# Kernel tuning notes

Measured on AMD Instinct MI355X. Metric: run time of the kernel, lower is better.

## Reference

```python
import jax, jax.numpy as jnp
import numpy as np

B, T, D_IN = 32, 1000, 1024
H = 32          # hidden_size
G = 4 * H       # gate dim (i,f,g,o)
L = 4           # num_layers


def setup_inputs() -> dict:
    key = jax.random.key(0)
    ks = jax.random.split(key, 12)
    s = 1.0 / np.sqrt(H)  # PyTorch LSTM init scale
    inp = {
        'x': jax.random.normal(ks[0], (B, T, D_IN), dtype=jnp.float32),
        # layer 0 (input dim 1024), [dir, ...]
        'w_ih0': jax.random.uniform(ks[1], (2, G, D_IN), minval=-s, maxval=s),
        'w_hh0': jax.random.uniform(ks[2], (2, G, H), minval=-s, maxval=s),
        'b_ih0': jax.random.uniform(ks[3], (2, G), minval=-s, maxval=s),
        'b_hh0': jax.random.uniform(ks[4], (2, G), minval=-s, maxval=s),
        # layers 1..3 (input dim 2H=64), [layer, dir, ...]
        'w_ih': jax.random.uniform(ks[5], (L - 1, 2, G, 2 * H), minval=-s, maxval=s),
        'w_hh': jax.random.uniform(ks[6], (L - 1, 2, G, H), minval=-s, maxval=s),
        'b_ih': jax.random.uniform(ks[7], (L - 1, 2, G), minval=-s, maxval=s),
        'b_hh': jax.random.uniform(ks[8], (L - 1, 2, G), minval=-s, maxval=s),
        # fc: Linear(64, 1)
        'fc_w': jax.random.uniform(ks[9], (1, 2 * H), minval=-0.125, maxval=0.125),
        'fc_b': jax.random.uniform(ks[10], (1,), minval=-0.125, maxval=0.125),
    }
    return inp


def _lstm_dir(x, wi, wh, b, reverse):
    # x: [B,T,Din]; wi: [4H,Din]; wh: [4H,H]; b: [4H]
    xp = jnp.einsum('btd,gd->tbg', x, wi) + b  # precomputed input proj [T,B,4H]
    whT = wh.T

    def step(carry, xt):
        h, c = carry
        g = xt + h @ whT
        i, f, gg, o = jnp.split(g, 4, axis=-1)  # PyTorch gate order i,f,g,o
        c = jax.nn.sigmoid(f) * c + jax.nn.sigmoid(i) * jnp.tanh(gg)
        h = jax.nn.sigmoid(o) * jnp.tanh(c)
        return (h, c), h

    init = (jnp.zeros((x.shape[0], H), x.dtype), jnp.zeros((x.shape[0], H), x.dtype))
    _, hs = jax.lax.scan(step, init, xp, reverse=reverse)  # hs aligned with input time order
    return hs.transpose(1, 0, 2)  # [B,T,H]


def _bilstm(x, wi, wh, bi, bh):
    fwd = _lstm_dir(x, wi[0], wh[0], bi[0] + bh[0], False)
    bwd = _lstm_dir(x, wi[1], wh[1], bi[1] + bh[1], True)
    return jnp.concatenate([fwd, bwd], axis=-1)  # [B,T,2H]


def reference(x, w_ih0, w_hh0, b_ih0, b_hh0, w_ih, w_hh, b_ih, b_hh, fc_w, fc_b):
    h = _bilstm(x, w_ih0, w_hh0, b_ih0, b_hh0)
    for l in range(L - 1):
        h = _bilstm(h, w_ih[l], w_hh[l], b_ih[l], b_hh[l])
    pooled = h.mean(axis=-2)           # [B,2H]
    return pooled @ fc_w.T + fc_b      # [B,1]
```

## Files before the change

kernel.cpp:

```cpp
#include <hip/hip_runtime.h>


#define TB 1000
#define LOG2E 1.44269504088896340736f

typedef int   v2i __attribute__((ext_vector_type(2)));
typedef float v2f __attribute__((ext_vector_type(2)));

__device__ __forceinline__ float fexp2(float x) {
#if __has_builtin(__builtin_amdgcn_exp2f)
    return __builtin_amdgcn_exp2f(x);
#else
    return exp2f(x);
#endif
}

__device__ __forceinline__ float lane_xor32(float v, bool pickx) {
    v2i r = __builtin_amdgcn_permlane32_swap(__float_as_int(v), __float_as_int(v),
                                             false, false);
    return __int_as_float(pickx ? r[0] : r[1]);
}

__global__ __launch_bounds__(256)
void gemm_proj(const float* __restrict__ A, int K,
               const float* __restrict__ W,
               const float* __restrict__ bi,
               const float* __restrict__ bh,
               float* __restrict__ xpT)
{
    __shared__ __align__(16) float As[32][68];
    __shared__ __align__(16) float Bs[32][132];

    const int tid = threadIdx.x;
    const int m0 = blockIdx.x * 64;
    const int n0 = blockIdx.y * 128;
    const int tx = tid & 15;
    const int ty = tid >> 4;

    float acc[8][4];
#pragma unroll
    for (int i = 0; i < 8; ++i)
#pragma unroll
        for (int jj = 0; jj < 4; ++jj) acc[i][jj] = 0.0f;

    const int ar = tid >> 3;
    const int ak = (tid & 7) * 4;
    const int wr = tid >> 1;
    const int wk = (tid & 1) * 16;

    for (int k0 = 0; k0 < K; k0 += 32) {
        float4 a0 = *(const float4*)(A + (size_t)(m0 + ar) * K + k0 + ak);
        float4 a1 = *(const float4*)(A + (size_t)(m0 + ar + 32) * K + k0 + ak);
        const float* wp = W + (size_t)(n0 + wr) * K + k0 + wk;
        float4 w0 = *(const float4*)(wp + 0);
        float4 w1 = *(const float4*)(wp + 4);
        float4 w2 = *(const float4*)(wp + 8);
        float4 w3 = *(const float4*)(wp + 12);

        __syncthreads();
        As[ak + 0][ar] = a0.x; As[ak + 1][ar] = a0.y;
        As[ak + 2][ar] = a0.z; As[ak + 3][ar] = a0.w;
        As[ak + 0][ar + 32] = a1.x; As[ak + 1][ar + 32] = a1.y;
        As[ak + 2][ar + 32] = a1.z; As[ak + 3][ar + 32] = a1.w;
        {
            float wv[16] = {w0.x, w0.y, w0.z, w0.w,
                            w1.x, w1.y, w1.z, w1.w,
                            w2.x, w2.y, w2.z, w2.w,
                            w3.x, w3.y, w3.z, w3.w};
#pragma unroll
            for (int q = 0; q < 16; ++q) Bs[wk + q][wr] = wv[q];
        }
        __syncthreads();

#pragma unroll
        for (int kk = 0; kk < 32; ++kk) {
            float4 av = *(const float4*)&As[kk][tx * 4];
            float4 b0 = *(const float4*)&Bs[kk][ty * 8];
            float4 b1 = *(const float4*)&Bs[kk][ty * 8 + 4];
            float bn[8] = {b0.x, b0.y, b0.z, b0.w, b1.x, b1.y, b1.z, b1.w};
#pragma unroll
            for (int ni = 0; ni < 8; ++ni) {
                acc[ni][0] = fmaf(av.x, bn[ni], acc[ni][0]);
                acc[ni][1] = fmaf(av.y, bn[ni], acc[ni][1]);
                acc[ni][2] = fmaf(av.z, bn[ni], acc[ni][2]);
                acc[ni][3] = fmaf(av.w, bn[ni], acc[ni][3]);
            }
        }
    }

    const int dir = n0 >> 7;
    const int mbase = m0 + tx * 4;
    const int bidx = mbase / 1000;
    const int ttq = mbase - bidx * 1000;
#pragma unroll
    for (int ni = 0; ni < 8; ++ni) {
        const int n = n0 + ty * 8 + ni;
        const float bias = bi[n] + bh[n];
        const float sc = (((n >> 5) & 3) == 2) ? (-2.0f * LOG2E) : (-LOG2E);
        float* row = xpT + ((size_t)((dir * 32 + bidx) * 128) + (n & 127)) * TB;
        if (dir == 0) {
            float4 o = {(acc[ni][0] + bias) * sc, (acc[ni][1] + bias) * sc,
                        (acc[ni][2] + bias) * sc, (acc[ni][3] + bias) * sc};
            *(float4*)(row + ttq) = o;
        } else {
            float4 o = {(acc[ni][3] + bias) * sc, (acc[ni][2] + bias) * sc,
                        (acc[ni][1] + bias) * sc, (acc[ni][0] + bias) * sc};
            *(float4*)(row + (TB - 4 - ttq)) = o;
        }
    }
}

template<int MODE>
__global__ __launch_bounds__(64)
void lstm_rec(const float* __restrict__ xpT,
              const float* __restrict__ whh,
              float* __restrict__ hout,
              float* __restrict__ hsum)
{
    __shared__ __align__(16) float hsh[32];

    const int blk  = blockIdx.x;
    const int dir  = blk >> 5;
    const int b    = blk & 31;
    const int lane = threadIdx.x & 63;
    const int j    = lane & 31;
    const int up   = lane >> 5;
    const int r0   = j + up * 64;
    const int r1   = r0 + 32;

    v2i det = __builtin_amdgcn_permlane32_swap(lane, lane, false, false);
    const bool pickx = (det[0] == (lane ^ 32));

    const float sA = up ? (-2.0f * LOG2E) : (-LOG2E);
    const float sB = -LOG2E;
    v2f wa[16], wb[16];
    {
        const float* wp0 = whh + (size_t)(dir * 128 + r0) * 32;
        const float* wp1 = whh + (size_t)(dir * 128 + r1) * 32;
#pragma unroll
        for (int q = 0; q < 8; ++q) {
            float4 v = *(const float4*)(wp0 + q * 4);
            wa[2 * q + 0][0] = v.x * sA; wa[2 * q + 0][1] = v.y * sA;
            wa[2 * q + 1][0] = v.z * sA; wa[2 * q + 1][1] = v.w * sA;
            float4 u = *(const float4*)(wp1 + q * 4);
            wb[2 * q + 0][0] = u.x * sB; wb[2 * q + 0][1] = u.y * sB;
            wb[2 * q + 1][0] = u.z * sB; wb[2 * q + 1][1] = u.w * sB;
        }
    }

    const float* pa = xpT + ((size_t)blk * 128 + r0) * TB;
    const float* pb = xpT + ((size_t)blk * 128 + r1) * TB;

    float4 A0 = *(const float4*)(pa + 0);
    float4 B0 = *(const float4*)(pb + 0);
    float4 A1 = *(const float4*)(pa + 4);
    float4 B1 = *(const float4*)(pb + 4);

    const float mA = up ?  2.0f : 1.0f;
    const float mB = up ? -1.0f : 0.0f;

    float c = 0.0f, h = 0.0f, hacc = 0.0f;
    float* hq = hout + ((size_t)b * TB + (dir ? TB - 1 : 0)) * 64 + dir * 32 + j;
    const int hstep = dir ? -64 : 64;

    const unsigned lds_z  = (unsigned)(size_t)&hsh[0];
    const unsigned lds_wa = lds_z + 4u * (unsigned)j;

    float4 hv0, hv1, hv2, hv3, hv4v, hv5, hv6, hv7;

#define DS_WRITE_H() \
    asm volatile("ds_write_b32 %0, %1" :: "v"(lds_wa), "v"(h))

#define DS_ISSUE_READS() do {                                                   \
    asm volatile("ds_read_b128 %0, %1 offset:0"   : "=v"(hv0)  : "v"(lds_z));   \
    asm volatile("ds_read_b128 %0, %1 offset:16"  : "=v"(hv1)  : "v"(lds_z));   \
    asm volatile("ds_read_b128 %0, %1 offset:32"  : "=v"(hv2)  : "v"(lds_z));   \
    asm volatile("ds_read_b128 %0, %1 offset:48"  : "=v"(hv3)  : "v"(lds_z));   \
    asm volatile("ds_read_b128 %0, %1 offset:64"  : "=v"(hv4v) : "v"(lds_z));   \
    asm volatile("ds_read_b128 %0, %1 offset:80"  : "=v"(hv5)  : "v"(lds_z));   \
    asm volatile("ds_read_b128 %0, %1 offset:96"  : "=v"(hv6)  : "v"(lds_z));   \
    asm volatile("ds_read_b128 %0, %1 offset:112" : "=v"(hv7)  : "v"(lds_z));   \
    } while (0)

#define MVG(HV, CNT, I0, I1, Q)                                                 \
    asm volatile("s_waitcnt lgkmcnt(" #CNT ")");                                \
    __builtin_amdgcn_sched_barrier(0);                                          \
    {                                                                           \
        v2f h0_ = {HV.x, HV.y};                                                 \
        v2f h1_ = {HV.z, HV.w};                                                 \
        qa[I0] = __builtin_elementwise_fma(h0_, wa[2*Q],   qa[I0]);             \
        qb[I0] = __builtin_elementwise_fma(h0_, wb[2*Q],   qb[I0]);             \
        qa[I1] = __builtin_elementwise_fma(h1_, wa[2*Q+1], qa[I1]);             \
        qb[I1] = __builtin_elementwise_fma(h1_, wb[2*Q+1], qb[I1]);             \
    }

    DS_WRITE_H();
    DS_ISSUE_READS();

#define LSTM_STEP(GA, GB) do {                                                  \
        v2f qa[4], qb[4];                                                       \
        qa[0] = v2f{(GA), 0.0f}; qa[1] = v2f{0.f, 0.f};                         \
        qa[2] = v2f{0.f, 0.f};   qa[3] = v2f{0.f, 0.f};                         \
        qb[0] = v2f{(GB), 0.0f}; qb[1] = v2f{0.f, 0.f};                         \
        qb[2] = v2f{0.f, 0.f};   qb[3] = v2f{0.f, 0.f};                         \
        MVG(hv0,  7, 0, 1, 0)                                                   \
        MVG(hv1,  6, 2, 3, 1)                                                   \
        MVG(hv2,  5, 0, 1, 2)                                                   \
        MVG(hv3,  4, 2, 3, 3)                                                   \
        MVG(hv4v, 3, 0, 1, 4)                                                   \
        MVG(hv5,  2, 2, 3, 5)                                                   \
        MVG(hv6,  1, 0, 1, 6)                                                   \
        MVG(hv7,  0, 2, 3, 7)                                                   \
        v2f sa = (qa[0] + qa[2]) + (qa[1] + qa[3]);                             \
        v2f sb = (qb[0] + qb[2]) + (qb[1] + qb[3]);                             \
        float g0 = sa[0] + sa[1];                                               \
        float g1 = sb[0] + sb[1];                                               \
        float s0 = __builtin_amdgcn_rcpf(1.0f + fexp2(g0));                     \
        float v0 = fmaf(mA, s0, mB);               \
        float v1 = __builtin_amdgcn_rcpf(1.0f + fexp2(g1));  \
        float o0 = lane_xor32(v0, pickx);                                       \
        float o1 = lane_xor32(v1, pickx);                                       \
        float P  = v0 * o0;                        \
        float sf = up ? o1 : v1;                                                \
        float so = up ? v1 : o1;                                                \
        c = fmaf(sf, c, P);                                                     \
        float tc = fmaf(2.0f, __builtin_amdgcn_rcpf(1.0f + fexp2(c * (-2.0f * LOG2E))), -1.0f); \
        h = so * tc;                                                            \
        DS_WRITE_H();                                                           \
        DS_ISSUE_READS();                                                       \
        if (MODE == 0) {                                                        \
            asm volatile("global_store_dword %0, %1, off" :: "v"(hq), "v"(h));  \
        } else {                                                                \
            hacc += h;                                                          \
        }                                                                       \
        hq += hstep;                                                            \
    } while (0)

    for (int it = 0; it < 125; ++it) {
        const int base = it * 8;
        const int offn0 = min(base + 8,  TB - 4);
        const int offn1 = min(base + 12, TB - 4);
        float4 NA0 = *(const float4*)(pa + offn0);
        float4 NB0 = *(const float4*)(pb + offn0);
        float4 NA1 = *(const float4*)(pa + offn1);
        float4 NB1 = *(const float4*)(pb + offn1);

        LSTM_STEP(A0.x, B0.x);
        LSTM_STEP(A0.y, B0.y);
        LSTM_STEP(A0.z, B0.z);
        LSTM_STEP(A0.w, B0.w);
        LSTM_STEP(A1.x, B1.x);
        LSTM_STEP(A1.y, B1.y);
        LSTM_STEP(A1.z, B1.z);
        LSTM_STEP(A1.w, B1.w);

        A0 = NA0; B0 = NB0; A1 = NA1; B1 = NB1;
    }
#undef LSTM_STEP
#undef MVG
#undef DS_ISSUE_READS
#undef DS_WRITE_H

    asm volatile("s_waitcnt lgkmcnt(0)" ::: "memory");

    if (MODE == 1) hsum[b * 64 + dir * 32 + j] = hacc;
}

__global__ __launch_bounds__(64)
void final_fc(const float* __restrict__ hsum,
              const float* __restrict__ fcw,
              const float* __restrict__ fcb,
              float* __restrict__ out)
{
    int b = blockIdx.x;
    int l = threadIdx.x;
    float v = hsum[b * 64 + l] * (1.0f / (float)TB) * fcw[l];
#pragma unroll
    for (int off = 32; off > 0; off >>= 1)
        v += __shfl_down(v, off, 64);
    if (l == 0) out[b] = v + fcb[0];
}

extern "C" void kernel_launch(void* const* d_in, const int* in_sizes, int n_in,
                              void* d_out, int out_size, void* d_ws, size_t ws_size,
                              hipStream_t stream)
{
    const float* x    = (const float*)d_in[0];
    const float* wih0 = (const float*)d_in[1];
    const float* whh0 = (const float*)d_in[2];
    const float* bih0 = (const float*)d_in[3];
    const float* bhh0 = (const float*)d_in[4];
    const float* wih  = (const float*)d_in[5];
    const float* whh  = (const float*)d_in[6];
    const float* bih  = (const float*)d_in[7];
    const float* bhh  = (const float*)d_in[8];
    const float* fcw  = (const float*)d_in[9];
    const float* fcb  = (const float*)d_in[10];
    float* out = (float*)d_out;

    float* ws = (float*)d_ws;
    float* xp = ws;
    float* hb = ws + 8192000;
    float* hs = ws + 8192000 + 2048000;

    dim3 gb(500, 2);

    gemm_proj<<<gb, 256, 0, stream>>>(x, 1024, wih0, bih0, bhh0, xp);
    lstm_rec<0><<<64, 64, 0, stream>>>(xp, whh0, hb, hs);

    for (int l = 1; l < 4; ++l) {
        const float* wl  = wih + (size_t)(l - 1) * 2 * 128 * 64;
        const float* whl = whh + (size_t)(l - 1) * 2 * 128 * 32;
        const float* b1  = bih + (size_t)(l - 1) * 256;
        const float* b2  = bhh + (size_t)(l - 1) * 256;
        gemm_proj<<<gb, 256, 0, stream>>>(hb, 64, wl, b1, b2, xp);
        if (l == 3) lstm_rec<1><<<64, 64, 0, stream>>>(xp, whl, hb, hs);
        else        lstm_rec<0><<<64, 64, 0, stream>>>(xp, whl, hb, hs);
    }

    final_fc<<<32, 64, 0, stream>>>(hs, fcw, fcb, out);
}
```

Baseline: 1.033 ms.

## Double-buffer projection GEMM and read first h lanes via readlane

The input-projection GEMM now uses two LDS buffers, so the next K-chunk's global loads overlap the current chunk's FMAs and one barrier per iteration is removed. In the recurrent LSTM step, the first 8 hidden values come from v_readlane of the wave's own h register into SGPRs and feed packed FMAs, replacing two LDS reads on the serial critical path. The aim is to shorten per-timestep latency. The inline asm clobbers fixed SGPRs s64-s71, and it relies on lanes 0-7 holding h[0..7]. That holds only if this wave produced those lanes.

```diff
diff --git a/kernel.cpp b/kernel.cpp
--- a/kernel.cpp
+++ b/kernel.cpp
@@ -28,8 +28,8 @@
                const float* __restrict__ bh,
                float* __restrict__ xpT)
 {
-    __shared__ __align__(16) float As[32][68];
-    __shared__ __align__(16) float Bs[32][132];
+    __shared__ __align__(16) float As[2][32][72];
+    __shared__ __align__(16) float Bs[2][32][132];
 
     const int tid = threadIdx.x;
     const int m0 = blockIdx.x * 64;
@@ -37,46 +37,54 @@
     const int tx = tid & 15;
     const int ty = tid >> 4;
 
-    float acc[8][4];
-#pragma unroll
-    for (int i = 0; i < 8; ++i)
-#pragma unroll
-        for (int jj = 0; jj < 4; ++jj) acc[i][jj] = 0.0f;
+    float acc[8][4] = {};
 
     const int ar = tid >> 3;
     const int ak = (tid & 7) * 4;
     const int wr = tid >> 1;
     const int wk = (tid & 1) * 16;
 
-    for (int k0 = 0; k0 < K; k0 += 32) {
-        float4 a0 = *(const float4*)(A + (size_t)(m0 + ar) * K + k0 + ak);
-        float4 a1 = *(const float4*)(A + (size_t)(m0 + ar + 32) * K + k0 + ak);
-        const float* wp = W + (size_t)(n0 + wr) * K + k0 + wk;
-        float4 w0 = *(const float4*)(wp + 0);
-        float4 w1 = *(const float4*)(wp + 4);
-        float4 w2 = *(const float4*)(wp + 8);
-        float4 w3 = *(const float4*)(wp + 12);
-
-        __syncthreads();
-        As[ak + 0][ar] = a0.x; As[ak + 1][ar] = a0.y;
-        As[ak + 2][ar] = a0.z; As[ak + 3][ar] = a0.w;
-        As[ak + 0][ar + 32] = a1.x; As[ak + 1][ar + 32] = a1.y;
-        As[ak + 2][ar + 32] = a1.z; As[ak + 3][ar + 32] = a1.w;
-        {
-            float wv[16] = {w0.x, w0.y, w0.z, w0.w,
-                            w1.x, w1.y, w1.z, w1.w,
-                            w2.x, w2.y, w2.z, w2.w,
-                            w3.x, w3.y, w3.z, w3.w};
-#pragma unroll
-            for (int q = 0; q < 16; ++q) Bs[wk + q][wr] = wv[q];
-        }
-        __syncthreads();
+    const float* Abase = A + (size_t)(m0 + ar) * K + ak;
+    const float* Wbase = W + (size_t)(n0 + wr) * K + wk;
+
+    float4 a0 = *(const float4*)(Abase);
+    float4 a1 = *(const float4*)(Abase + (size_t)32 * K);
+    float4 w0 = *(const float4*)(Wbase + 0);
+    float4 w1 = *(const float4*)(Wbase + 4);
+    float4 w2 = *(const float4*)(Wbase + 8);
+    float4 w3 = *(const float4*)(Wbase + 12);
+
+    {
+        As[0][ak + 0][ar] = a0.x; As[0][ak + 1][ar] = a0.y;
+        As[0][ak + 2][ar] = a0.z; As[0][ak + 3][ar] = a0.w;
+        As[0][ak + 0][ar + 32] = a1.x; As[0][ak + 1][ar + 32] = a1.y;
+        As[0][ak + 2][ar + 32] = a1.z; As[0][ak + 3][ar + 32] = a1.w;
+        float wv[16] = {w0.x, w0.y, w0.z, w0.w, w1.x, w1.y, w1.z, w1.w,
+                        w2.x, w2.y, w2.z, w2.w, w3.x, w3.y, w3.z, w3.w};
+#pragma unroll
+        for (int q = 0; q < 16; ++q) Bs[0][wk + q][wr] = wv[q];
+    }
+    __syncthreads();
+
+    const int nch = K >> 5;
+    int p = 0;
+    for (int ch = 0; ch < nch; ++ch) {
+        const bool more = (ch + 1 < nch);
+        if (more) {
+            const int k0 = (ch + 1) * 32;
+            a0 = *(const float4*)(Abase + k0);
+            a1 = *(const float4*)(Abase + (size_t)32 * K + k0);
+            w0 = *(const float4*)(Wbase + k0);
+            w1 = *(const float4*)(Wbase + k0 + 4);
+            w2 = *(const float4*)(Wbase + k0 + 8);
+            w3 = *(const float4*)(Wbase + k0 + 12);
+        }
 
 #pragma unroll
         for (int kk = 0; kk < 32; ++kk) {
-            float4 av = *(const float4*)&As[kk][tx * 4];
-            float4 b0 = *(const float4*)&Bs[kk][ty * 8];
-            float4 b1 = *(const float4*)&Bs[kk][ty * 8 + 4];
+            float4 av = *(const float4*)&As[p][kk][tx * 4];
+            float4 b0 = *(const float4*)&Bs[p][kk][ty * 8];
+            float4 b1 = *(const float4*)&Bs[p][kk][ty * 8 + 4];
             float bn[8] = {b0.x, b0.y, b0.z, b0.w, b1.x, b1.y, b1.z, b1.w};
 #pragma unroll
             for (int ni = 0; ni < 8; ++ni) {
@@ -86,6 +94,20 @@
                 acc[ni][3] = fmaf(av.w, bn[ni], acc[ni][3]);
             }
         }
+
+        if (more) {
+            const int np = p ^ 1;
+            As[np][ak + 0][ar] = a0.x; As[np][ak + 1][ar] = a0.y;
+            As[np][ak + 2][ar] = a0.z; As[np][ak + 3][ar] = a0.w;
+            As[np][ak + 0][ar + 32] = a1.x; As[np][ak + 1][ar + 32] = a1.y;
+            As[np][ak + 2][ar + 32] = a1.z; As[np][ak + 3][ar + 32] = a1.w;
+            float wv[16] = {w0.x, w0.y, w0.z, w0.w, w1.x, w1.y, w1.z, w1.w,
+                            w2.x, w2.y, w2.z, w2.w, w3.x, w3.y, w3.z, w3.w};
+#pragma unroll
+            for (int q = 0; q < 16; ++q) Bs[np][wk + q][wr] = wv[q];
+            __syncthreads();
+        }
+        p ^= 1;
     }
 
     const int dir = n0 >> 7;
@@ -166,14 +188,12 @@
     const unsigned lds_z  = (unsigned)(size_t)&hsh[0];
     const unsigned lds_wa = lds_z + 4u * (unsigned)j;
 
-    float4 hv0, hv1, hv2, hv3, hv4v, hv5, hv6, hv7;
+    float4 hv2, hv3, hv4v, hv5, hv6, hv7;
 
 #define DS_WRITE_H() \
     asm volatile("ds_write_b32 %0, %1" :: "v"(lds_wa), "v"(h))
 
 #define DS_ISSUE_READS() do {                                                   \
-    asm volatile("ds_read_b128 %0, %1 offset:0"   : "=v"(hv0)  : "v"(lds_z));   \
-    asm volatile("ds_read_b128 %0, %1 offset:16"  : "=v"(hv1)  : "v"(lds_z));   \
     asm volatile("ds_read_b128 %0, %1 offset:32"  : "=v"(hv2)  : "v"(lds_z));   \
     asm volatile("ds_read_b128 %0, %1 offset:48"  : "=v"(hv3)  : "v"(lds_z));   \
     asm volatile("ds_read_b128 %0, %1 offset:64"  : "=v"(hv4v) : "v"(lds_z));   \
@@ -182,37 +202,59 @@
     asm volatile("ds_read_b128 %0, %1 offset:112" : "=v"(hv7)  : "v"(lds_z));   \
     } while (0)
 
-#define MVG(HV, CNT, I0, I1, Q)                                                 \
+#define RLPK01() do {                                                           \
+    asm volatile(                                                               \
+        "v_readlane_b32 s64, %8, 0\n\t"                                         \
+        "v_readlane_b32 s65, %8, 1\n\t"                                         \
+        "v_readlane_b32 s66, %8, 2\n\t"                                         \
+        "v_readlane_b32 s67, %8, 3\n\t"                                         \
+        "v_readlane_b32 s68, %8, 4\n\t"                                         \
+        "v_readlane_b32 s69, %8, 5\n\t"                                         \
+        "v_readlane_b32 s70, %8, 6\n\t"                                         \
+        "v_readlane_b32 s71, %8, 7\n\t"                                         \
+        "v_pk_fma_f32 %0, s[64:65], %9, %0\n\t"                                 \
+        "v_pk_fma_f32 %1, s[64:65], %10, %1\n\t"                                \
+        "v_pk_fma_f32 %2, s[66:67], %11, %2\n\t"                                \
+        "v_pk_fma_f32 %3, s[66:67], %12, %3\n\t"                                \
+        "v_pk_fma_f32 %4, s[68:69], %13, %4\n\t"                                \
+        "v_pk_fma_f32 %5, s[68:69], %14, %5\n\t"                                \
+        "v_pk_fma_f32 %6, s[70:71], %15, %6\n\t"                                \
+        "v_pk_fma_f32 %7, s[70:71], %16, %7"                                    \
+        : "+v"(qa0), "+v"(qb0), "+v"(qa1), "+v"(qb1),                           \
+          "+v"(qa2), "+v"(qb2), "+v"(qa3), "+v"(qb3)                            \
+        : "v"(__float_as_int(h)),                                               \
+          "v"(wa[0]), "v"(wb[0]), "v"(wa[1]), "v"(wb[1]),                       \
+          "v"(wa[2]), "v"(wb[2]), "v"(wa[3]), "v"(wb[3])                        \
+        : "s64","s65","s66","s67","s68","s69","s70","s71");                     \
+    } while (0)
+
+#define MVG(HV, CNT, QA0, QB0, QA1, QB1, Q)                                     \
     asm volatile("s_waitcnt lgkmcnt(" #CNT ")");                                \
     __builtin_amdgcn_sched_barrier(0);                                          \
     {                                                                           \
         v2f h0_ = {HV.x, HV.y};                                                 \
         v2f h1_ = {HV.z, HV.w};                                                 \
-        qa[I0] = __builtin_elementwise_fma(h0_, wa[2*Q],   qa[I0]);             \
-        qb[I0] = __builtin_elementwise_fma(h0_, wb[2*Q],   qb[I0]);             \
-        qa[I1] = __builtin_elementwise_fma(h1_, wa[2*Q+1], qa[I1]);             \
-        qb[I1] = __builtin_elementwise_fma(h1_, wb[2*Q+1], qb[I1]);             \
+        QA0 = __builtin_elementwise_fma(h0_, wa[2*Q],   QA0);                   \
+        QB0 = __builtin_elementwise_fma(h0_, wb[2*Q],   QB0);                   \
+        QA1 = __builtin_elementwise_fma(h1_, wa[2*Q+1], QA1);                   \
+        QB1 = __builtin_elementwise_fma(h1_, wb[2*Q+1], QB1);                   \
     }
 
     DS_WRITE_H();
     DS_ISSUE_READS();
 
 #define LSTM_STEP(GA, GB) do {                                                  \
-        v2f qa[4], qb[4];                                                       \
-        qa[0] = v2f{(GA), 0.0f}; qa[1] = v2f{0.f, 0.f};                         \
-        qa[2] = v2f{0.f, 0.f};   qa[3] = v2f{0.f, 0.f};                         \
-        qb[0] = v2f{(GB), 0.0f}; qb[1] = v2f{0.f, 0.f};                         \
-        qb[2] = v2f{0.f, 0.f};   qb[3] = v2f{0.f, 0.f};                         \
-        MVG(hv0,  7, 0, 1, 0)                                                   \
-        MVG(hv1,  6, 2, 3, 1)                                                   \
-        MVG(hv2,  5, 0, 1, 2)                                                   \
-        MVG(hv3,  4, 2, 3, 3)                                                   \
-        MVG(hv4v, 3, 0, 1, 4)                                                   \
-        MVG(hv5,  2, 2, 3, 5)                                                   \
-        MVG(hv6,  1, 0, 1, 6)                                                   \
-        MVG(hv7,  0, 2, 3, 7)                                                   \
-        v2f sa = (qa[0] + qa[2]) + (qa[1] + qa[3]);                             \
-        v2f sb = (qb[0] + qb[2]) + (qb[1] + qb[3]);                             \
+        v2f qa0 = {(GA), 0.0f}, qa1 = {0.f,0.f}, qa2 = {0.f,0.f}, qa3 = {0.f,0.f}; \
+        v2f qb0 = {(GB), 0.0f}, qb1 = {0.f,0.f}, qb2 = {0.f,0.f}, qb3 = {0.f,0.f}; \
+        RLPK01();                                                               \
+        MVG(hv2,  5, qa0, qb0, qa1, qb1, 2)                                     \
+        MVG(hv3,  4, qa2, qb2, qa3, qb3, 3)                                     \
+        MVG(hv4v, 3, qa0, qb0, qa1, qb1, 4)                                     \
+        MVG(hv5,  2, qa2, qb2, qa3, qb3, 5)                                     \
+        MVG(hv6,  1, qa0, qb0, qa1, qb1, 6)                                     \
+        MVG(hv7,  0, qa2, qb2, qa3, qb3, 7)                                     \
+        v2f sa = (qa0 + qa2) + (qa1 + qa3);                                     \
+        v2f sb = (qb0 + qb2) + (qb1 + qb3);                                     \
         float g0 = sa[0] + sa[1];                                               \
         float g1 = sb[0] + sb[1];                                               \
         float s0 = __builtin_amdgcn_rcpf(1.0f + fexp2(g0));                     \
@@ -258,6 +300,7 @@
     }
 #undef LSTM_STEP
 #undef MVG
+#undef RLPK01
 #undef DS_ISSUE_READS
 #undef DS_WRITE_H
 
```

Measured after the change: 1.295 ms. 1.25x slower.

## Enlarge projection GEMM tile to 128x128 with register-prefetched global loads

Applied to the files above, without the earlier changes.

The input-projection GEMM now computes a 128x128 output tile per block, so each thread holds an 8x8 accumulator instead of 8x4 and reuses each shared-memory value more often. The next K-chunk is loaded into registers while the current chunk is being computed, which hides global-load latency. The cost is higher register pressure and half as many blocks (250x2), which may reduce occupancy on the large GPU. The epilogue is rewritten so each thread writes two float4 time-segments per gate column.

```diff
diff --git a/kernel.cpp b/kernel.cpp
--- a/kernel.cpp
+++ b/kernel.cpp
@@ -28,84 +28,111 @@
                const float* __restrict__ bh,
                float* __restrict__ xpT)
 {
-    __shared__ __align__(16) float As[32][68];
-    __shared__ __align__(16) float Bs[32][132];
+    __shared__ __align__(16) float As[32][132];
+    __shared__ __align__(16) float Ws[32][132];
 
     const int tid = threadIdx.x;
-    const int m0 = blockIdx.x * 64;
+    const int m0 = blockIdx.x * 128;
     const int n0 = blockIdx.y * 128;
     const int tx = tid & 15;
     const int ty = tid >> 4;
 
-    float acc[8][4];
-#pragma unroll
-    for (int i = 0; i < 8; ++i)
-#pragma unroll
-        for (int jj = 0; jj < 4; ++jj) acc[i][jj] = 0.0f;
-
-    const int ar = tid >> 3;
-    const int ak = (tid & 7) * 4;
-    const int wr = tid >> 1;
-    const int wk = (tid & 1) * 16;
-
-    for (int k0 = 0; k0 < K; k0 += 32) {
-        float4 a0 = *(const float4*)(A + (size_t)(m0 + ar) * K + k0 + ak);
-        float4 a1 = *(const float4*)(A + (size_t)(m0 + ar + 32) * K + k0 + ak);
-        const float* wp = W + (size_t)(n0 + wr) * K + k0 + wk;
-        float4 w0 = *(const float4*)(wp + 0);
-        float4 w1 = *(const float4*)(wp + 4);
-        float4 w2 = *(const float4*)(wp + 8);
-        float4 w3 = *(const float4*)(wp + 12);
+    float acc[8][8] = {};
+
+    const int row = tid >> 1;
+    const int kq  = (tid & 1) * 16;
+
+    const float* Ab = A + (size_t)(m0 + row) * K + kq;
+    const float* Wb = W + (size_t)(n0 + row) * K + kq;
+
+    float4 pa0 = *(const float4*)(Ab + 0);
+    float4 pa1 = *(const float4*)(Ab + 4);
+    float4 pa2 = *(const float4*)(Ab + 8);
+    float4 pa3 = *(const float4*)(Ab + 12);
+    float4 pw0 = *(const float4*)(Wb + 0);
+    float4 pw1 = *(const float4*)(Wb + 4);
+    float4 pw2 = *(const float4*)(Wb + 8);
+    float4 pw3 = *(const float4*)(Wb + 12);
+
+#define STAGE() do {                                                            \
+        float av_[16] = {pa0.x,pa0.y,pa0.z,pa0.w, pa1.x,pa1.y,pa1.z,pa1.w,      \
+                         pa2.x,pa2.y,pa2.z,pa2.w, pa3.x,pa3.y,pa3.z,pa3.w};     \
+        float wv_[16] = {pw0.x,pw0.y,pw0.z,pw0.w, pw1.x,pw1.y,pw1.z,pw1.w,      \
+                         pw2.x,pw2.y,pw2.z,pw2.w, pw3.x,pw3.y,pw3.z,pw3.w};     \
+        _Pragma("unroll")                                                       \
+        for (int q = 0; q < 16; ++q) As[kq + q][row] = av_[q];                  \
+        _Pragma("unroll")                                                       \
+        for (int q = 0; q < 16; ++q) Ws[kq + q][row] = wv_[q];                  \
+    } while (0)
+
+    STAGE();
+    __syncthreads();
+
+    const int nch = K >> 5;
+    for (int ch = 0; ch < nch; ++ch) {
+        const bool more = (ch + 1 < nch);
+        if (more) {
+            const int k0 = (ch + 1) * 32;
+            pa0 = *(const float4*)(Ab + k0 + 0);
+            pa1 = *(const float4*)(Ab + k0 + 4);
+            pa2 = *(const float4*)(Ab + k0 + 8);
+            pa3 = *(const float4*)(Ab + k0 + 12);
+            pw0 = *(const float4*)(Wb + k0 + 0);
+            pw1 = *(const float4*)(Wb + k0 + 4);
+            pw2 = *(const float4*)(Wb + k0 + 8);
+            pw3 = *(const float4*)(Wb + k0 + 12);
+        }
+
+#pragma unroll
+        for (int kk = 0; kk < 32; ++kk) {
+            float4 a0 = *(const float4*)&As[kk][ty * 8];
+            float4 a1 = *(const float4*)&As[kk][ty * 8 + 4];
+            float4 w0 = *(const float4*)&Ws[kk][tx * 8];
+            float4 w1 = *(const float4*)&Ws[kk][tx * 8 + 4];
+            float am[8] = {a0.x, a0.y, a0.z, a0.w, a1.x, a1.y, a1.z, a1.w};
+            float wn[8] = {w0.x, w0.y, w0.z, w0.w, w1.x, w1.y, w1.z, w1.w};
+#pragma unroll
+            for (int mi = 0; mi < 8; ++mi)
+#pragma unroll
+                for (int ni = 0; ni < 8; ++ni)
+                    acc[mi][ni] = fmaf(am[mi], wn[ni], acc[mi][ni]);
+        }
 
         __syncthreads();
-        As[ak + 0][ar] = a0.x; As[ak + 1][ar] = a0.y;
-        As[ak + 2][ar] = a0.z; As[ak + 3][ar] = a0.w;
-        As[ak + 0][ar + 32] = a1.x; As[ak + 1][ar + 32] = a1.y;
-        As[ak + 2][ar + 32] = a1.z; As[ak + 3][ar + 32] = a1.w;
-        {
-            float wv[16] = {w0.x, w0.y, w0.z, w0.w,
-                            w1.x, w1.y, w1.z, w1.w,
-                            w2.x, w2.y, w2.z, w2.w,
-                            w3.x, w3.y, w3.z, w3.w};
-#pragma unroll
-            for (int q = 0; q < 16; ++q) Bs[wk + q][wr] = wv[q];
-        }
-        __syncthreads();
-
-#pragma unroll
-        for (int kk = 0; kk < 32; ++kk) {
-            float4 av = *(const float4*)&As[kk][tx * 4];
-            float4 b0 = *(const float4*)&Bs[kk][ty * 8];
-            float4 b1 = *(const float4*)&Bs[kk][ty * 8 + 4];
-            float bn[8] = {b0.x, b0.y, b0.z, b0.w, b1.x, b1.y, b1.z, b1.w};
-#pragma unroll
-            for (int ni = 0; ni < 8; ++ni) {
-                acc[ni][0] = fmaf(av.x, bn[ni], acc[ni][0]);
-                acc[ni][1] = fmaf(av.y, bn[ni], acc[ni][1]);
-                acc[ni][2] = fmaf(av.z, bn[ni], acc[ni][2]);
-                acc[ni][3] = fmaf(av.w, bn[ni], acc[ni][3]);
-            }
-        }
-    }
+        if (more) {
+            STAGE();
+            __syncthreads();
+        }
+    }
+#undef STAGE
 
     const int dir = n0 >> 7;
-    const int mbase = m0 + tx * 4;
-    const int bidx = mbase / 1000;
-    const int ttq = mbase - bidx * 1000;
+    const int mb = m0 + ty * 8;
 #pragma unroll
     for (int ni = 0; ni < 8; ++ni) {
-        const int n = n0 + ty * 8 + ni;
+        const int n = n0 + tx * 8 + ni;
         const float bias = bi[n] + bh[n];
         const float sc = (((n >> 5) & 3) == 2) ? (-2.0f * LOG2E) : (-LOG2E);
-        float* row = xpT + ((size_t)((dir * 32 + bidx) * 128) + (n & 127)) * TB;
-        if (dir == 0) {
-            float4 o = {(acc[ni][0] + bias) * sc, (acc[ni][1] + bias) * sc,
-                        (acc[ni][2] + bias) * sc, (acc[ni][3] + bias) * sc};
-            *(float4*)(row + ttq) = o;
-        } else {
-            float4 o = {(acc[ni][3] + bias) * sc, (acc[ni][2] + bias) * sc,
-                        (acc[ni][1] + bias) * sc, (acc[ni][0] + bias) * sc};
-            *(float4*)(row + (TB - 4 - ttq)) = o;
+        float* rowp = xpT + ((size_t)((dir * 32) * 128) + (n & 127)) * TB;
+#pragma unroll
+        for (int qd = 0; qd < 2; ++qd) {
+            const int mq = mb + qd * 4;
+            const int bidx = mq / 1000;
+            const int ttq = mq - bidx * 1000;
+            float* rp = rowp + (size_t)bidx * 128 * TB;
+            if (dir == 0) {
+                float4 o = {(acc[qd*4+0][ni] + bias) * sc,
+                            (acc[qd*4+1][ni] + bias) * sc,
+                            (acc[qd*4+2][ni] + bias) * sc,
+                            (acc[qd*4+3][ni] + bias) * sc};
+                *(float4*)(rp + ttq) = o;
+            } else {
+                float4 o = {(acc[qd*4+3][ni] + bias) * sc,
+                            (acc[qd*4+2][ni] + bias) * sc,
+                            (acc[qd*4+1][ni] + bias) * sc,
+                            (acc[qd*4+0][ni] + bias) * sc};
+                *(float4*)(rp + (TB - 4 - ttq)) = o;
+            }
         }
     }
 }
@@ -303,7 +330,7 @@
     float* hb = ws + 8192000;
     float* hs = ws + 8192000 + 2048000;
 
-    dim3 gb(500, 2);
+    dim3 gb(250, 2);
 
     gemm_proj<<<gb, 256, 0, stream>>>(x, 1024, wih0, bih0, bhh0, xp);
     lstm_rec<0><<<64, 64, 0, stream>>>(xp, whh0, hb, hs);
```

Result: slower. 2.069 ms (+100.3%).
